# Kernel optimization log

Measured on AMD Instinct MI355X. Metric: run time of the kernel, lower is better.

Reference implementation:

```python
import jax, jax.numpy as jnp
import numpy as np

N_NODES = 100000
N_EDGES = 1600000
IN_DIM, HID_DIM, OUT_DIM = 128, 128, 64


def gcn_conv(x, W, b, src, dst, n_nodes):
    # PyG GCNConv: h = X W; out = D^-1/2 (A + I) D^-1/2 h + b
    h = x @ W  # [N, F_out]
    ones = jnp.ones(src.shape[0], dtype=h.dtype)
    deg = jax.ops.segment_sum(ones, dst, num_segments=n_nodes) + 1.0  # +1 self-loop
    dinv = jax.lax.rsqrt(deg)  # deg >= 1, no division by zero
    norm = dinv[src] * dinv[dst]  # [E]
    msg = h[src] * norm[:, None]  # [E, F_out] gather + scale
    agg = jax.ops.segment_sum(msg, dst, num_segments=n_nodes)  # scatter-add
    # self-loop contribution: h_i * dinv_i^2
    agg = agg + h * (dinv * dinv)[:, None]
    return agg + b


def setup_inputs() -> dict:
    key = jax.random.key(0)
    ks = jax.random.split(key, 9)
    x = jax.random.normal(ks[0], (N_NODES, IN_DIM), dtype=jnp.float32)
    edge_index = jax.random.randint(ks[1], (2, N_EDGES), 0, N_NODES, dtype=jnp.int64 if jax.config.jax_enable_x64 else jnp.int32)
    s = 1.0 / np.sqrt(IN_DIM)
    W1 = jax.random.uniform(ks[2], (IN_DIM, HID_DIM), jnp.float32, -s, s)
    b1 = jax.random.uniform(ks[3], (HID_DIM,), jnp.float32, -s, s)
    sh = 1.0 / np.sqrt(HID_DIM)
    W2 = jax.random.uniform(ks[4], (HID_DIM, HID_DIM), jnp.float32, -sh, sh)
    b2 = jax.random.uniform(ks[5], (HID_DIM,), jnp.float32, -sh, sh)
    Wfc = jax.random.uniform(ks[6], (HID_DIM, OUT_DIM), jnp.float32, -sh, sh)
    bfc = jax.random.uniform(ks[7], (OUT_DIM,), jnp.float32, -sh, sh)
    return {"x": x, "edge_index": edge_index, "W1": W1, "b1": b1,
            "W2": W2, "b2": b2, "Wfc": Wfc, "bfc": bfc}


def reference(x, edge_index, W1, b1, W2, b2, Wfc, bfc):
    src, dst = edge_index[0], edge_index[1]
    n = x.shape[0]
    h = jax.nn.relu(gcn_conv(x, W1, b1, src, dst, n))
    h = jax.nn.relu(gcn_conv(h, W2, b2, src, dst, n))
    return h @ Wfc + bfc
```

## Files before the change

### kernel.cpp

```cpp
#include <hip/hip_runtime.h>

typedef unsigned int uint;
typedef unsigned short ushort;

__device__ inline ushort f2bf(float f) {
  uint u = __float_as_uint(f);
  u += 0x7fffu + ((u >> 16) & 1u);
  return (ushort)(u >> 16);
}
__device__ inline float bf_lo(uint u) { return __uint_as_float(u << 16); }
__device__ inline float bf_hi(uint u) { return __uint_as_float(u & 0xffff0000u); }


__global__ __launch_bounds__(256) void hist_kernel(const int* __restrict__ dst,
                                                   int* __restrict__ deg, int nE) {
  int i = blockIdx.x * 256 + threadIdx.x;
  int stride = gridDim.x * 256;
  for (; i < nE; i += stride) atomicAdd(&deg[dst[i]], 1);
}

__global__ __launch_bounds__(256) void scan1(const int* __restrict__ deg,
                                             int* __restrict__ row_off,
                                             int* __restrict__ blocksums, int n) {
  __shared__ int s[256];
  int t = threadIdx.x, i = blockIdx.x * 256 + t;
  int v = (i < n) ? deg[i] : 0;
  s[t] = v;
  __syncthreads();
  for (int off = 1; off < 256; off <<= 1) {
    int x = (t >= off) ? s[t - off] : 0;
    __syncthreads();
    s[t] += x;
    __syncthreads();
  }
  if (i < n) row_off[i] = s[t] - v;
  if (t == 255) blocksums[blockIdx.x] = s[t];
}

__global__ __launch_bounds__(512) void scan2(int* __restrict__ blocksums, int nb,
                                             int* __restrict__ total_out) {
  __shared__ int s[512];
  int t = threadIdx.x;
  int v = (t < nb) ? blocksums[t] : 0;
  s[t] = v;
  __syncthreads();
  for (int off = 1; off < 512; off <<= 1) {
    int x = (t >= off) ? s[t - off] : 0;
    __syncthreads();
    s[t] += x;
    __syncthreads();
  }
  if (t < nb) blocksums[t] = s[t] - v;
  if (t == 511) *total_out = s[511];
}

__global__ __launch_bounds__(256) void scan3_dinv(int* __restrict__ row_off,
                                                  const int* __restrict__ blockoff,
                                                  const int* __restrict__ deg,
                                                  float* __restrict__ dinv, int n) {
  int i = blockIdx.x * 256 + threadIdx.x;
  if (i < n) {
    row_off[i] += blockoff[i >> 8];
    dinv[i] = rsqrtf((float)deg[i] + 1.0f);
  }
}

__global__ __launch_bounds__(256) void scatter_kernel(const int* __restrict__ src,
                                                      const int* __restrict__ dst,
                                                      const int* __restrict__ row_off,
                                                      int* __restrict__ cursor,
                                                      int* __restrict__ edge_src, int nE,
                                                      int lo, int hi) {
  int i = blockIdx.x * 256 + threadIdx.x;
  int stride = gridDim.x * 256;
  for (; i < nE; i += stride) {
    int d = dst[i];
    if (d >= lo && d < hi) {
      int pos = row_off[d] + atomicAdd(&cursor[d], 1);
      edge_src[pos] = src[i];
    }
  }
}

template <int COLS, bool BIAS, bool RELU, bool OUT_BF16>
__global__ __launch_bounds__(256) void gemm_k128(const float* __restrict__ X,
                                                 const float* __restrict__ W,
                                                 const float* __restrict__ bias,
                                                 void* __restrict__ Yv, int nrows) {
  constexpr int TN = COLS / 16;
  __shared__ float Xs[128][33];
  __shared__ float Ws[32 * COLS];
  int tid = threadIdx.x;
  int ty = tid >> 4, tx = tid & 15;
  long row0 = (long)blockIdx.x * 128;

  float acc[8][TN];
#pragma unroll
  for (int r = 0; r < 8; ++r)
#pragma unroll
    for (int j = 0; j < TN; ++j) acc[r][j] = 0.f;

  for (int kt = 0; kt < 4; ++kt) {
#pragma unroll
    for (int l = 0; l < 4; ++l) {
      int idx = tid + l * 256;
      int r = idx >> 3;
      int k4 = (idx & 7) << 2;
      float4 v = make_float4(0.f, 0.f, 0.f, 0.f);
      long gr = row0 + r;
      if (gr < nrows) v = *(const float4*)(X + gr * 128 + kt * 32 + k4);
      Xs[r][k4 + 0] = v.x;
      Xs[r][k4 + 1] = v.y;
      Xs[r][k4 + 2] = v.z;
      Xs[r][k4 + 3] = v.w;
    }
    constexpr int WF4 = 32 * COLS / 4;
#pragma unroll
    for (int l = 0; l < WF4 / 256; ++l) {
      int idx = tid + l * 256;
      float4 v = *(const float4*)(W + (size_t)kt * 32 * COLS + (size_t)idx * 4);
      *(float4*)(&Ws[idx * 4]) = v;
    }
    __syncthreads();
#pragma unroll
    for (int kk = 0; kk < 32; ++kk) {
      float a[8];
#pragma unroll
      for (int r = 0; r < 8; ++r) a[r] = Xs[ty * 8 + r][kk];
      float b[TN];
      float4 b0 = *(const float4*)(&Ws[kk * COLS + tx * 4]);
      b[0] = b0.x; b[1] = b0.y; b[2] = b0.z; b[3] = b0.w;
      if constexpr (TN == 8) {
        float4 b1 = *(const float4*)(&Ws[kk * COLS + 64 + tx * 4]);
        b[4] = b1.x; b[5] = b1.y; b[6] = b1.z; b[7] = b1.w;
      }
#pragma unroll
      for (int r = 0; r < 8; ++r)
#pragma unroll
        for (int j = 0; j < TN; ++j) acc[r][j] = fmaf(a[r], b[j], acc[r][j]);
    }
    __syncthreads();
  }

  float bv[TN];
  if constexpr (BIAS) {
#pragma unroll
    for (int j = 0; j < TN; ++j) {
      int col = (j < 4) ? tx * 4 + j : 64 + tx * 4 + (j - 4);
      bv[j] = bias[col];
    }
  }
#pragma unroll
  for (int r = 0; r < 8; ++r) {
    long row = row0 + ty * 8 + r;
    if (row < nrows) {
#pragma unroll
      for (int j = 0; j < TN; ++j) {
        if constexpr (BIAS) acc[r][j] += bv[j];
        if constexpr (RELU) acc[r][j] = fmaxf(acc[r][j], 0.f);
      }
      if constexpr (OUT_BF16) {
        ushort* Yb = (ushort*)Yv;
        ushort4 o;
        o.x = f2bf(acc[r][0]); o.y = f2bf(acc[r][1]);
        o.z = f2bf(acc[r][2]); o.w = f2bf(acc[r][3]);
        *(ushort4*)(Yb + (size_t)row * COLS + tx * 4) = o;
        if constexpr (TN == 8) {
          ushort4 o2;
          o2.x = f2bf(acc[r][4]); o2.y = f2bf(acc[r][5]);
          o2.z = f2bf(acc[r][6]); o2.w = f2bf(acc[r][7]);
          *(ushort4*)(Yb + (size_t)row * COLS + 64 + tx * 4) = o2;
        }
      } else {
        float* Y = (float*)Yv;
        float4 o = make_float4(acc[r][0], acc[r][1], acc[r][2], acc[r][3]);
        *(float4*)(Y + (size_t)row * COLS + tx * 4) = o;
        if constexpr (TN == 8) {
          float4 o2 = make_float4(acc[r][4], acc[r][5], acc[r][6], acc[r][7]);
          *(float4*)(Y + (size_t)row * COLS + 64 + tx * 4) = o2;
        }
      }
    }
  }
}

__global__ __launch_bounds__(128) void agg_kernel(const ushort* __restrict__ H,
                                                  const int* __restrict__ row_off,
                                                  const int* __restrict__ edge_src,
                                                  const float* __restrict__ dinv,
                                                  const float* __restrict__ bias,
                                                  float* __restrict__ Out, int n) {
  int i = blockIdx.x;
  int t = threadIdx.x;
  int g = t >> 4;
  int c = t & 15;
  float di = dinv[i];
  int beg = row_off[i], end = row_off[i + 1];

  float acc[8];
#pragma unroll
  for (int k = 0; k < 8; ++k) acc[k] = 0.f;

  __shared__ int sidx[128];
  __shared__ float swt[128];
  for (int base = beg; base < end; base += 128) {
    int cnt = min(128, end - base);
    if (t < cnt) {
      int s = edge_src[base + t];
      sidx[t] = s;
      swt[t] = dinv[s] * di;
    }
    __syncthreads();
#pragma unroll 2
    for (int j = g; j < cnt; j += 8) {
      uint4 q = *(const uint4*)(H + (size_t)sidx[j] * 128 + c * 8);
      float w = swt[j];
      acc[0] = fmaf(bf_lo(q.x), w, acc[0]);
      acc[1] = fmaf(bf_hi(q.x), w, acc[1]);
      acc[2] = fmaf(bf_lo(q.y), w, acc[2]);
      acc[3] = fmaf(bf_hi(q.y), w, acc[3]);
      acc[4] = fmaf(bf_lo(q.z), w, acc[4]);
      acc[5] = fmaf(bf_hi(q.z), w, acc[5]);
      acc[6] = fmaf(bf_lo(q.w), w, acc[6]);
      acc[7] = fmaf(bf_hi(q.w), w, acc[7]);
    }
    __syncthreads();
  }

#pragma unroll
  for (int k = 0; k < 8; ++k) acc[k] += __shfl_down(acc[k], 32);
#pragma unroll
  for (int k = 0; k < 8; ++k) acc[k] += __shfl_down(acc[k], 16);

  __shared__ float red[16][8];
  if (t >= 64 && t < 80) {
#pragma unroll
    for (int k = 0; k < 8; ++k) red[c][k] = acc[k];
  }
  __syncthreads();
  if (t < 16) {
    uint4 q = *(const uint4*)(H + (size_t)i * 128 + c * 8);
    float sw = di * di;
    float self_[8] = {bf_lo(q.x), bf_hi(q.x), bf_lo(q.y), bf_hi(q.y),
                      bf_lo(q.z), bf_hi(q.z), bf_lo(q.w), bf_hi(q.w)};
    float4 bA = *(const float4*)(bias + c * 8);
    float4 bB = *(const float4*)(bias + c * 8 + 4);
    float o[8];
#pragma unroll
    for (int k = 0; k < 8; ++k) o[k] = acc[k] + red[c][k] + self_[k] * sw;
    o[0] += bA.x; o[1] += bA.y; o[2] += bA.z; o[3] += bA.w;
    o[4] += bB.x; o[5] += bB.y; o[6] += bB.z; o[7] += bB.w;
#pragma unroll
    for (int k = 0; k < 8; ++k) o[k] = fmaxf(o[k], 0.f);
    *(float4*)(Out + (size_t)i * 128 + c * 8) = make_float4(o[0], o[1], o[2], o[3]);
    *(float4*)(Out + (size_t)i * 128 + c * 8 + 4) = make_float4(o[4], o[5], o[6], o[7]);
  }
}


extern "C" void kernel_launch(void* const* d_in, const int* in_sizes, int n_in,
                              void* d_out, int out_size, void* d_ws, size_t ws_size,
                              hipStream_t stream) {
  const float* x = (const float*)d_in[0];
  const int* ei = (const int*)d_in[1];
  const float* W1 = (const float*)d_in[2];
  const float* b1 = (const float*)d_in[3];
  const float* W2 = (const float*)d_in[4];
  const float* b2 = (const float*)d_in[5];
  const float* Wfc = (const float*)d_in[6];
  const float* bfc = (const float*)d_in[7];
  float* out = (float*)d_out;

  int N = in_sizes[0] / 128;
  int E = in_sizes[1] / 2;
  const int* srcp = ei;
  const int* dstp = ei + E;

  char* ws = (char*)d_ws;
  size_t off = 0;
  auto alloc = [&](size_t bytes) -> void* {
    void* p = ws + off;
    off += (bytes + 255) & ~(size_t)255;
    return p;
  };
  ushort* Hb = (ushort*)alloc((size_t)N * 128 * 2);
  float* X2 = (float*)alloc((size_t)N * 128 * 4);
  int* deg = (int*)alloc((size_t)N * 4);
  int* row_off = (int*)alloc((size_t)(N + 1) * 4);
  int* cursor = (int*)alloc((size_t)N * 4);
  int* blocksums = (int*)alloc(512 * 4);
  float* dinv = (float*)alloc((size_t)N * 4);
  int* edge_src = (int*)alloc((size_t)E * 4);

  hipMemsetAsync(deg, 0, (size_t)N * 4, stream);
  hipMemsetAsync(cursor, 0, (size_t)N * 4, stream);

  int nbE = (E + 255) / 256;
  if (nbE > 2048) nbE = 2048;
  hist_kernel<<<nbE, 256, 0, stream>>>(dstp, deg, E);

  int nbScan = (N + 255) / 256;
  scan1<<<nbScan, 256, 0, stream>>>(deg, row_off, blocksums, N);
  scan2<<<1, 512, 0, stream>>>(blocksums, nbScan, row_off + N);
  scan3_dinv<<<nbScan, 256, 0, stream>>>(row_off, blocksums, deg, dinv, N);

  constexpr int NPASS = 4;
  int wsz = (N + NPASS - 1) / NPASS;
  for (int w = 0; w < NPASS; ++w) {
    int lo = w * wsz;
    int hi = min(N, lo + wsz);
    scatter_kernel<<<nbE, 256, 0, stream>>>(srcp, dstp, row_off, cursor, edge_src, E, lo, hi);
  }

  int nbG = (N + 127) / 128;
  gemm_k128<128, false, false, true><<<nbG, 256, 0, stream>>>(x, W1, nullptr, Hb, N);
  agg_kernel<<<N, 128, 0, stream>>>(Hb, row_off, edge_src, dinv, b1, X2, N);
  gemm_k128<128, false, false, true><<<nbG, 256, 0, stream>>>(X2, W2, nullptr, Hb, N);
  agg_kernel<<<N, 128, 0, stream>>>(Hb, row_off, edge_src, dinv, b2, X2, N);
  gemm_k128<64, true, false, false><<<nbG, 256, 0, stream>>>(X2, Wfc, bfc, out, N);
}
```

Measured before the change: 565.9 us.

## Replace FP32 SIMT GEMMs with split-bf16 MFMA GEMMs

New measurement: 569.4 us. No clear change (+0.6%).

```diff
diff --git a/kernel.cpp b/kernel.cpp
--- a/kernel.cpp
+++ b/kernel.cpp
@@ -2,14 +2,23 @@
 
 typedef unsigned int uint;
 typedef unsigned short ushort;
+
+typedef short bf16x8 __attribute__((ext_vector_type(8)));
+typedef float f32x4 __attribute__((ext_vector_type(4)));
 
 __device__ inline ushort f2bf(float f) {
   uint u = __float_as_uint(f);
   u += 0x7fffu + ((u >> 16) & 1u);
   return (ushort)(u >> 16);
 }
+__device__ inline float bf2f(ushort h) { return __uint_as_float((uint)h << 16); }
 __device__ inline float bf_lo(uint u) { return __uint_as_float(u << 16); }
 __device__ inline float bf_hi(uint u) { return __uint_as_float(u & 0xffff0000u); }
+__device__ inline void split2(float v, ushort& h, ushort& l) {
+  ushort hh = f2bf(v);
+  h = hh;
+  l = f2bf(v - bf2f(hh));
+}
 
 
 __global__ __launch_bounds__(256) void hist_kernel(const int* __restrict__ dst,
@@ -82,106 +91,105 @@
   }
 }
 
-template <int COLS, bool BIAS, bool RELU, bool OUT_BF16>
-__global__ __launch_bounds__(256) void gemm_k128(const float* __restrict__ X,
-                                                 const float* __restrict__ W,
+
+__global__ __launch_bounds__(256) void split_x_kernel(const float* __restrict__ X,
+                                                      ushort* __restrict__ Xhi,
+                                                      ushort* __restrict__ Xlo, int n4) {
+  int i = blockIdx.x * 256 + threadIdx.x;
+  int stride = gridDim.x * 256;
+  for (; i < n4; i += stride) {
+    float4 v = *(const float4*)(X + (size_t)i * 4);
+    ushort4 h, l;
+    split2(v.x, h.x, l.x);
+    split2(v.y, h.y, l.y);
+    split2(v.z, h.z, l.z);
+    split2(v.w, h.w, l.w);
+    *(ushort4*)(Xhi + (size_t)i * 4) = h;
+    *(ushort4*)(Xlo + (size_t)i * 4) = l;
+  }
+}
+
+__global__ __launch_bounds__(256) void split_wT_kernel(const float* __restrict__ W,
+                                                       ushort* __restrict__ WThi,
+                                                       ushort* __restrict__ WTlo, int C) {
+  int idx = blockIdx.x * 256 + threadIdx.x;
+  if (idx < 128 * C) {
+    int k = idx / C, c = idx % C;
+    ushort h, l;
+    split2(W[idx], h, l);
+    WThi[c * 128 + k] = h;
+    WTlo[c * 128 + k] = l;
+  }
+}
+
+template <int COLS, bool OUT_BF16>
+__global__ __launch_bounds__(256) void gemm_mfma(const ushort* __restrict__ Ahi,
+                                                 const ushort* __restrict__ Alo,
+                                                 const ushort* __restrict__ WThi,
+                                                 const ushort* __restrict__ WTlo,
                                                  const float* __restrict__ bias,
                                                  void* __restrict__ Yv, int nrows) {
-  constexpr int TN = COLS / 16;
-  __shared__ float Xs[128][33];
-  __shared__ float Ws[32 * COLS];
+  constexpr int NCF = COLS / 16;
   int tid = threadIdx.x;
-  int ty = tid >> 4, tx = tid & 15;
-  long row0 = (long)blockIdx.x * 128;
-
-  float acc[8][TN];
-#pragma unroll
-  for (int r = 0; r < 8; ++r)
-#pragma unroll
-    for (int j = 0; j < TN; ++j) acc[r][j] = 0.f;
-
-  for (int kt = 0; kt < 4; ++kt) {
-#pragma unroll
-    for (int l = 0; l < 4; ++l) {
-      int idx = tid + l * 256;
-      int r = idx >> 3;
-      int k4 = (idx & 7) << 2;
-      float4 v = make_float4(0.f, 0.f, 0.f, 0.f);
-      long gr = row0 + r;
-      if (gr < nrows) v = *(const float4*)(X + gr * 128 + kt * 32 + k4);
-      Xs[r][k4 + 0] = v.x;
-      Xs[r][k4 + 1] = v.y;
-      Xs[r][k4 + 2] = v.z;
-      Xs[r][k4 + 3] = v.w;
-    }
-    constexpr int WF4 = 32 * COLS / 4;
-#pragma unroll
-    for (int l = 0; l < WF4 / 256; ++l) {
-      int idx = tid + l * 256;
-      float4 v = *(const float4*)(W + (size_t)kt * 32 * COLS + (size_t)idx * 4);
-      *(float4*)(&Ws[idx * 4]) = v;
-    }
-    __syncthreads();
-#pragma unroll
-    for (int kk = 0; kk < 32; ++kk) {
-      float a[8];
-#pragma unroll
-      for (int r = 0; r < 8; ++r) a[r] = Xs[ty * 8 + r][kk];
-      float b[TN];
-      float4 b0 = *(const float4*)(&Ws[kk * COLS + tx * 4]);
-      b[0] = b0.x; b[1] = b0.y; b[2] = b0.z; b[3] = b0.w;
-      if constexpr (TN == 8) {
-        float4 b1 = *(const float4*)(&Ws[kk * COLS + 64 + tx * 4]);
-        b[4] = b1.x; b[5] = b1.y; b[6] = b1.z; b[7] = b1.w;
+  int w = tid >> 6;
+  int lane = tid & 63;
+  int lrow = lane & 15;
+  int k0 = (lane >> 4) * 8;
+  long row0 = (long)blockIdx.x * 128 + w * 32;
+
+  f32x4 acc[2][NCF];
+#pragma unroll
+  for (int rf = 0; rf < 2; ++rf)
+#pragma unroll
+    for (int cf = 0; cf < NCF; ++cf) acc[rf][cf] = (f32x4){0.f, 0.f, 0.f, 0.f};
+
+  const bf16x8 zero8 = {0, 0, 0, 0, 0, 0, 0, 0};
+#pragma unroll
+  for (int ks = 0; ks < 4; ++ks) {
+    int kk = ks * 32 + k0;
+    bf16x8 a_hi[2], a_lo[2];
+#pragma unroll
+    for (int rf = 0; rf < 2; ++rf) {
+      long r = row0 + rf * 16 + lrow;
+      bool ok = r < nrows;
+      a_hi[rf] = ok ? *(const bf16x8*)(Ahi + r * 128 + kk) : zero8;
+      a_lo[rf] = ok ? *(const bf16x8*)(Alo + r * 128 + kk) : zero8;
+    }
+    bf16x8 b_hi[NCF], b_lo[NCF];
+#pragma unroll
+    for (int cf = 0; cf < NCF; ++cf) {
+      int c = cf * 16 + lrow;
+      b_hi[cf] = *(const bf16x8*)(WThi + c * 128 + kk);
+      b_lo[cf] = *(const bf16x8*)(WTlo + c * 128 + kk);
+    }
+#pragma unroll
+    for (int rf = 0; rf < 2; ++rf)
+#pragma unroll
+      for (int cf = 0; cf < NCF; ++cf) {
+        acc[rf][cf] = __builtin_amdgcn_mfma_f32_16x16x32_bf16(a_hi[rf], b_hi[cf], acc[rf][cf], 0, 0, 0);
+        acc[rf][cf] = __builtin_amdgcn_mfma_f32_16x16x32_bf16(a_hi[rf], b_lo[cf], acc[rf][cf], 0, 0, 0);
+        acc[rf][cf] = __builtin_amdgcn_mfma_f32_16x16x32_bf16(a_lo[rf], b_hi[cf], acc[rf][cf], 0, 0, 0);
       }
-#pragma unroll
-      for (int r = 0; r < 8; ++r)
-#pragma unroll
-        for (int j = 0; j < TN; ++j) acc[r][j] = fmaf(a[r], b[j], acc[r][j]);
-    }
-    __syncthreads();
-  }
-
-  float bv[TN];
-  if constexpr (BIAS) {
-#pragma unroll
-    for (int j = 0; j < TN; ++j) {
-      int col = (j < 4) ? tx * 4 + j : 64 + tx * 4 + (j - 4);
-      bv[j] = bias[col];
-    }
-  }
-#pragma unroll
-  for (int r = 0; r < 8; ++r) {
-    long row = row0 + ty * 8 + r;
-    if (row < nrows) {
-#pragma unroll
-      for (int j = 0; j < TN; ++j) {
-        if constexpr (BIAS) acc[r][j] += bv[j];
-        if constexpr (RELU) acc[r][j] = fmaxf(acc[r][j], 0.f);
-      }
-      if constexpr (OUT_BF16) {
-        ushort* Yb = (ushort*)Yv;
-        ushort4 o;
-        o.x = f2bf(acc[r][0]); o.y = f2bf(acc[r][1]);
-        o.z = f2bf(acc[r][2]); o.w = f2bf(acc[r][3]);
-        *(ushort4*)(Yb + (size_t)row * COLS + tx * 4) = o;
-        if constexpr (TN == 8) {
-          ushort4 o2;
-          o2.x = f2bf(acc[r][4]); o2.y = f2bf(acc[r][5]);
-          o2.z = f2bf(acc[r][6]); o2.w = f2bf(acc[r][7]);
-          *(ushort4*)(Yb + (size_t)row * COLS + 64 + tx * 4) = o2;
-        }
-      } else {
-        float* Y = (float*)Yv;
-        float4 o = make_float4(acc[r][0], acc[r][1], acc[r][2], acc[r][3]);
-        *(float4*)(Y + (size_t)row * COLS + tx * 4) = o;
-        if constexpr (TN == 8) {
-          float4 o2 = make_float4(acc[r][4], acc[r][5], acc[r][6], acc[r][7]);
-          *(float4*)(Y + (size_t)row * COLS + 64 + tx * 4) = o2;
+  }
+
+  int rbase = (lane >> 4) * 4;
+#pragma unroll
+  for (int rf = 0; rf < 2; ++rf)
+#pragma unroll
+    for (int r = 0; r < 4; ++r) {
+      long row = row0 + rf * 16 + rbase + r;
+      if (row < nrows) {
+#pragma unroll
+        for (int cf = 0; cf < NCF; ++cf) {
+          int col = cf * 16 + lrow;
+          if constexpr (OUT_BF16) {
+            ((ushort*)Yv)[row * COLS + col] = f2bf(acc[rf][cf][r]);
+          } else {
+            ((float*)Yv)[row * COLS + col] = acc[rf][cf][r] + bias[col];
+          }
         }
       }
     }
-  }
 }
 
 __global__ __launch_bounds__(128) void agg_kernel(const ushort* __restrict__ H,
@@ -189,7 +197,8 @@
                                                   const int* __restrict__ edge_src,
                                                   const float* __restrict__ dinv,
                                                   const float* __restrict__ bias,
-                                                  float* __restrict__ Out, int n) {
+                                                  ushort* __restrict__ Ohi,
+                                                  ushort* __restrict__ Olo, int n) {
   int i = blockIdx.x;
   int t = threadIdx.x;
   int g = t >> 4;
@@ -250,10 +259,17 @@
     for (int k = 0; k < 8; ++k) o[k] = acc[k] + red[c][k] + self_[k] * sw;
     o[0] += bA.x; o[1] += bA.y; o[2] += bA.z; o[3] += bA.w;
     o[4] += bB.x; o[5] += bB.y; o[6] += bB.z; o[7] += bB.w;
+    ushort4 h0, h1, l0, l1;
 #pragma unroll
     for (int k = 0; k < 8; ++k) o[k] = fmaxf(o[k], 0.f);
-    *(float4*)(Out + (size_t)i * 128 + c * 8) = make_float4(o[0], o[1], o[2], o[3]);
-    *(float4*)(Out + (size_t)i * 128 + c * 8 + 4) = make_float4(o[4], o[5], o[6], o[7]);
+    split2(o[0], h0.x, l0.x); split2(o[1], h0.y, l0.y);
+    split2(o[2], h0.z, l0.z); split2(o[3], h0.w, l0.w);
+    split2(o[4], h1.x, l1.x); split2(o[5], h1.y, l1.y);
+    split2(o[6], h1.z, l1.z); split2(o[7], h1.w, l1.w);
+    *(ushort4*)(Ohi + (size_t)i * 128 + c * 8) = h0;
+    *(ushort4*)(Ohi + (size_t)i * 128 + c * 8 + 4) = h1;
+    *(ushort4*)(Olo + (size_t)i * 128 + c * 8) = l0;
+    *(ushort4*)(Olo + (size_t)i * 128 + c * 8 + 4) = l1;
   }
 }
 
@@ -284,7 +300,14 @@
     return p;
   };
   ushort* Hb = (ushort*)alloc((size_t)N * 128 * 2);
-  float* X2 = (float*)alloc((size_t)N * 128 * 4);
+  ushort* Xhi = (ushort*)alloc((size_t)N * 128 * 2);
+  ushort* Xlo = (ushort*)alloc((size_t)N * 128 * 2);
+  ushort* W1hiT = (ushort*)alloc(128 * 128 * 2);
+  ushort* W1loT = (ushort*)alloc(128 * 128 * 2);
+  ushort* W2hiT = (ushort*)alloc(128 * 128 * 2);
+  ushort* W2loT = (ushort*)alloc(128 * 128 * 2);
+  ushort* WfhiT = (ushort*)alloc(128 * 64 * 2);
+  ushort* WfloT = (ushort*)alloc(128 * 64 * 2);
   int* deg = (int*)alloc((size_t)N * 4);
   int* row_off = (int*)alloc((size_t)(N + 1) * 4);
   int* cursor = (int*)alloc((size_t)N * 4);
@@ -295,6 +318,11 @@
   hipMemsetAsync(deg, 0, (size_t)N * 4, stream);
   hipMemsetAsync(cursor, 0, (size_t)N * 4, stream);
 
+  split_x_kernel<<<2048, 256, 0, stream>>>(x, Xhi, Xlo, N * 32);
+  split_wT_kernel<<<(128 * 128 + 255) / 256, 256, 0, stream>>>(W1, W1hiT, W1loT, 128);
+  split_wT_kernel<<<(128 * 128 + 255) / 256, 256, 0, stream>>>(W2, W2hiT, W2loT, 128);
+  split_wT_kernel<<<(128 * 64 + 255) / 256, 256, 0, stream>>>(Wfc, WfhiT, WfloT, 64);
+
   int nbE = (E + 255) / 256;
   if (nbE > 2048) nbE = 2048;
   hist_kernel<<<nbE, 256, 0, stream>>>(dstp, deg, E);
@@ -313,9 +341,9 @@
   }
 
   int nbG = (N + 127) / 128;
-  gemm_k128<128, false, false, true><<<nbG, 256, 0, stream>>>(x, W1, nullptr, Hb, N);
-  agg_kernel<<<N, 128, 0, stream>>>(Hb, row_off, edge_src, dinv, b1, X2, N);
-  gemm_k128<128, false, false, true><<<nbG, 256, 0, stream>>>(X2, W2, nullptr, Hb, N);
-  agg_kernel<<<N, 128, 0, stream>>>(Hb, row_off, edge_src, dinv, b2, X2, N);
-  gemm_k128<64, true, false, false><<<nbG, 256, 0, stream>>>(X2, Wfc, bfc, out, N);
-}
+  gemm_mfma<128, true><<<nbG, 256, 0, stream>>>(Xhi, Xlo, W1hiT, W1loT, nullptr, Hb, N);
+  agg_kernel<<<N, 128, 0, stream>>>(Hb, row_off, edge_src, dinv, b1, Xhi, Xlo, N);
+  gemm_mfma<128, true><<<nbG, 256, 0, stream>>>(Xhi, Xlo, W2hiT, W2loT, nullptr, Hb, N);
+  agg_kernel<<<N, 128, 0, stream>>>(Hb, row_off, edge_src, dinv, b2, Xhi, Xlo, N);
+  gemm_mfma<64, false><<<nbG, 256, 0, stream>>>(Xhi, Xlo, WfhiT, WfloT, bfc, out, N);
+}
```
